# Kernel tuning notes

Hardware: AMD Instinct MI355X
Metric: run time of the kernel (lower is better)

Reference implementation:

```python
import jax, jax.numpy as jnp
import numpy as np

B, S, D, H = 2, 2048, 1024, 16
HD = D // H  # head dim = 64


def setup_inputs() -> dict:
    key = jax.random.key(0)
    ks = jax.random.split(key, 12)
    s = 1.0 / np.sqrt(D)
    return {
        "query": jax.random.normal(ks[0], (B, S, D), jnp.float32),
        "key": jax.random.normal(ks[1], (B, S, D), jnp.float32),
        "value": jax.random.normal(ks[2], (B, S, D), jnp.float32),
        "mask": jax.random.randint(ks[3], (B, S, S), 0, 2, jnp.int32),
        "wq_kernel": jax.random.normal(ks[4], (D, D), jnp.float32) * s,
        "wq_bias": jnp.zeros((D,), jnp.float32),
        "wk_kernel": jax.random.normal(ks[5], (D, D), jnp.float32) * s,
        "wk_bias": jnp.zeros((D,), jnp.float32),
        "wv_kernel": jax.random.normal(ks[6], (D, D), jnp.float32) * s,
        "wv_bias": jnp.zeros((D,), jnp.float32),
        "wo_kernel": jax.random.normal(ks[7], (D, D), jnp.float32) * s,
        "wo_bias": jnp.zeros((D,), jnp.float32),
    }


def reference(query, key, value, mask,
              wq_kernel, wq_bias, wk_kernel, wk_bias,
              wv_kernel, wv_bias, wo_kernel, wo_bias):
    b = query.shape[0]
    # Dense projections, then split heads: [B,S,D] -> [B,H,S,HD]
    def split_heads(x):
        return x.reshape(b, -1, H, HD).transpose(0, 2, 1, 3)

    q = split_heads(query @ wq_kernel + wq_bias)
    k = split_heads(key @ wk_kernel + wk_bias)
    v = split_heads(value @ wv_kernel + wv_bias)

    scores = jnp.einsum('bhqd,bhkd->bhqk', q, k) / jnp.sqrt(jnp.float32(HD))
    m = mask[:, None, :, :]  # [B,1,S,S] broadcast over heads
    scores = jnp.where(m == 0, jnp.float32(-1e9), scores)
    attn = jax.nn.softmax(scores, axis=-1)
    out = jnp.einsum('bhqk,bhkd->bhqd', attn, v)
    out = out.transpose(0, 2, 1, 3).reshape(b, -1, D)  # [B,S,D]
    return out @ wo_kernel + wo_bias
```

## Files before the change

### kernel.cpp

```cpp
#include <hip/hip_runtime.h>
#include <hip/hip_bf16.h>

typedef __attribute__((ext_vector_type(8))) short bf16x8;
typedef __attribute__((ext_vector_type(4))) float f32x4;
typedef __attribute__((ext_vector_type(16))) float f32x16;
typedef __attribute__((ext_vector_type(4))) unsigned int u32x4;
typedef unsigned long long u64;
typedef unsigned short u16;
typedef unsigned int u32;

#define LOG2E 1.44269504088896340736f

__device__ __forceinline__ u16 f2bf(float f) {
  u32 u = __builtin_bit_cast(u32, f);
  u32 r = u + 0x7FFFu + ((u >> 16) & 1u);
  return (u16)(r >> 16);
}

__device__ __forceinline__ u32 cvt_pk_bf16(float lo, float hi) {
  u32 r;
  asm("v_cvt_pk_bf16_f32 %0, %1, %2" : "=v"(r) : "v"(lo), "v"(hi));
  return r;
}

__device__ __forceinline__ void swap32(u32& a, u32& b) {
  asm("v_permlane32_swap_b32 %0, %1" : "+v"(a), "+v"(b));
}

__device__ __forceinline__ float fexp2(float x) {
#if __has_builtin(__builtin_amdgcn_exp2f)
  return __builtin_amdgcn_exp2f(x);
#else
  return exp2f(x);
#endif
}

__device__ __forceinline__ void gload16(const u16* g, u16* l) {
  __builtin_amdgcn_global_load_lds(
      (const __attribute__((address_space(1))) u32*)g,
      (__attribute__((address_space(3))) u32*)l, 16, 0, 0);
}

__global__ __launch_bounds__(256) void mask_bits(const int* __restrict__ mask,
                                                 u64* __restrict__ out) {
  const int nwords = 2 * 2048 * 32;
  int gw = (blockIdx.x * 256 + threadIdx.x) >> 6;
  int lane = threadIdx.x & 63;
  int nw = (gridDim.x * 256) >> 6;
  for (int w = gw; w < nwords; w += nw) {
    int m = mask[(size_t)w * 64 + lane];
    u64 bits = __ballot(m != 0);
    if (lane == 0) out[w] = bits;
  }
}

__global__ __launch_bounds__(256) void wtrans(const float* __restrict__ W0,
                                              const float* __restrict__ W1,
                                              const float* __restrict__ W2,
                                              const float* __restrict__ W3,
                                              u16* __restrict__ WtBase) {
  const float* W = (blockIdx.z == 0) ? W0 : (blockIdx.z == 1) ? W1
                    : (blockIdx.z == 2) ? W2 : W3;
  u16* T = WtBase + (size_t)blockIdx.z * 1048576;
  __shared__ float tile[32][33];
  int k0 = blockIdx.y * 32, n0 = blockIdx.x * 32;
  int tx = threadIdx.x, ty = threadIdx.y;
#pragma unroll
  for (int i = 0; i < 4; i++)
    tile[ty + i * 8][tx] = W[(size_t)(k0 + ty + i * 8) * 1024 + n0 + tx];
  __syncthreads();
#pragma unroll
  for (int i = 0; i < 4; i++)
    T[(size_t)(n0 + ty + i * 8) * 1024 + k0 + tx] = f2bf(tile[tx][ty + i * 8]);
}

__global__ __launch_bounds__(256) void vtrans(const u16* __restrict__ Vb,
                                              u16* __restrict__ Vt) {
  __shared__ u16 t[64][72];
  int bh = blockIdx.y, k0 = blockIdx.x * 64;
  const u16* src = Vb + (size_t)bh * 2048 * 64;
  u16* dst = Vt + (size_t)bh * 64 * 2048;
  int tid = threadIdx.x;
  int r = tid >> 2, c = (tid & 3) * 16;
  *(bf16x8*)&t[r][c] = *(const bf16x8*)(src + (size_t)(k0 + r) * 64 + c);
  *(bf16x8*)&t[r][c + 8] = *(const bf16x8*)(src + (size_t)(k0 + r) * 64 + c + 8);
  __syncthreads();
  int d = tid >> 2, kb = (tid & 3) * 16;
  u16 tmp[16];
#pragma unroll
  for (int i = 0; i < 16; i++) tmp[i] = t[kb + i][d];
  *(bf16x8*)(dst + (size_t)d * 2048 + k0 + kb) = *(bf16x8*)&tmp[0];
  *(bf16x8*)(dst + (size_t)d * 2048 + k0 + kb + 8) = *(bf16x8*)&tmp[8];
}

__global__ __launch_bounds__(256, 3) void gemm_qkv(
    const float* __restrict__ Aq, const float* __restrict__ Ak,
    const float* __restrict__ Av, const float* __restrict__ bq,
    const float* __restrict__ bk, const float* __restrict__ bv,
    const u16* __restrict__ WtBase, u16* __restrict__ OutBase) {
  constexpr int K = 1024;
  __shared__ alignas(16) u16 As[128][40];
  __shared__ alignas(16) u16 Bs[2][128][32];
  const int fid = blockIdx.x;
  const int c = fid & 7, i = fid >> 3;
  const int panel = c * 12 + (i >> 3);
  const int my = panel & 31, z = panel >> 5;
  const int m0 = my * 128, n0 = (i & 7) * 128;

  const float* A = (z == 0) ? Aq : (z == 1) ? Ak : Av;
  const float* bias = (z == 0) ? bq : (z == 1) ? bk : bv;
  const u16* Bt = WtBase + (size_t)z * 1048576;
  u16* Ob = OutBase + (size_t)z * 4194304;
  const float scale = (z == 0) ? 0.125f * LOG2E : 1.0f;

  const int tid = threadIdx.x;
  const int lane = tid & 63, wave = tid >> 6;
  const int wr = wave >> 1, wc = wave & 1;
  const int fr = lane & 15, fq = lane >> 4;

  const int arow = tid >> 1, ahalf = tid & 1;
  const float* Agp = A + (size_t)(m0 + arow) * K + ahalf * 16;
  const int srow = lane >> 2, scol = (lane & 3) * 8;
  const u16* Bgp = Bt + (size_t)(n0 + wave * 32 + srow) * K + scol;

  f32x4 acc[4][4];
#pragma unroll
  for (int i2 = 0; i2 < 4; i2++)
#pragma unroll
    for (int j = 0; j < 4; j++) acc[i2][j] = (f32x4){0.f, 0.f, 0.f, 0.f};

  gload16(Bgp, &Bs[0][wave * 32][0]);
  gload16(Bgp + 16 * K, &Bs[0][wave * 32 + 16][0]);
  float4 a0 = *(const float4*)(Agp);
  float4 a1 = *(const float4*)(Agp + 4);
  float4 a2 = *(const float4*)(Agp + 8);
  float4 a3 = *(const float4*)(Agp + 12);

  for (int k0 = 0; k0 < K; k0 += 32) {
    const int cur = (k0 >> 5) & 1;
    __builtin_amdgcn_sched_barrier(0);
    __builtin_amdgcn_s_barrier();
    __builtin_amdgcn_sched_barrier(0);
    u32 c0 = cvt_pk_bf16(a0.x, a0.y), c1 = cvt_pk_bf16(a0.z, a0.w);
    u32 c2 = cvt_pk_bf16(a1.x, a1.y), c3 = cvt_pk_bf16(a1.z, a1.w);
    u32 c4 = cvt_pk_bf16(a2.x, a2.y), c5 = cvt_pk_bf16(a2.z, a2.w);
    u32 c6 = cvt_pk_bf16(a3.x, a3.y), c7 = cvt_pk_bf16(a3.z, a3.w);
    *(u32x4*)&As[arow][ahalf * 16] = (u32x4){c0, c1, c2, c3};
    *(u32x4*)&As[arow][ahalf * 16 + 8] = (u32x4){c4, c5, c6, c7};
    if (k0 + 32 < K) {
      gload16(Bgp + k0 + 32, &Bs[cur ^ 1][wave * 32][0]);
      gload16(Bgp + k0 + 32 + 16 * K, &Bs[cur ^ 1][wave * 32 + 16][0]);
    }
    asm volatile("s_waitcnt lgkmcnt(0)" ::: "memory");
    __builtin_amdgcn_sched_barrier(0);
    __builtin_amdgcn_s_barrier();
    __builtin_amdgcn_sched_barrier(0);
    if (k0 + 32 < K) {
      a0 = *(const float4*)(Agp + k0 + 32);
      a1 = *(const float4*)(Agp + k0 + 36);
      a2 = *(const float4*)(Agp + k0 + 40);
      a3 = *(const float4*)(Agp + k0 + 44);
    }
    bf16x8 af[4], bfv[4];
#pragma unroll
    for (int i2 = 0; i2 < 4; i2++) {
      af[i2] = *(const bf16x8*)&As[wr * 64 + i2 * 16 + fr][fq * 8];
      bfv[i2] = *(const bf16x8*)&Bs[cur][wc * 64 + i2 * 16 + fr][fq * 8];
    }
#pragma unroll
    for (int i2 = 0; i2 < 4; i2++)
#pragma unroll
      for (int j = 0; j < 4; j++)
        acc[i2][j] = __builtin_amdgcn_mfma_f32_16x16x32_bf16(af[i2], bfv[j],
                                                             acc[i2][j], 0, 0, 0);
  }
#pragma unroll
  for (int j = 0; j < 4; j++) {
    int col = n0 + wc * 64 + j * 16 + fr;
    float bcol = bias[col];
    int hh = col >> 6, hd = col & 63;
#pragma unroll
    for (int i2 = 0; i2 < 4; i2++) {
#pragma unroll
      for (int r = 0; r < 4; r++) {
        int row = m0 + wr * 64 + i2 * 16 + fq * 4 + r;
        int bb = row >> 11, ss = row & 2047;
        float val = (acc[i2][j][r] + bcol) * scale;
        Ob[(((size_t)bb * 16 + hh) * 2048 + ss) * 64 + hd] = f2bf(val);
      }
    }
  }
}

__global__ __launch_bounds__(256, 2) void gemm_out(const u16* __restrict__ A,
                                                   const u16* __restrict__ Bt,
                                                   const float* __restrict__ bias,
                                                   float* __restrict__ Out) {
  constexpr int K = 1024;
  __shared__ alignas(16) u16 As[64][32];
  __shared__ alignas(16) u16 Bs[128][32];
  const int fid = blockIdx.x;
  const int c = fid & 7, i = fid >> 3;
  const int panel = c * 8 + (i >> 3);
  const int m0 = panel * 64, n0 = (i & 7) * 128;

  const int tid = threadIdx.x;
  const int lane = tid & 63, wave = tid >> 6;
  const int wr = wave >> 1, wc = wave & 1;
  const int fr = lane & 15, fq = lane >> 4;

  const int srow = lane >> 2, scol = (lane & 3) * 8;
  const u16* Agp = A + (size_t)(m0 + wave * 16 + srow) * K + scol;
  const u16* Bgp = Bt + (size_t)(n0 + wave * 32 + srow) * K + scol;
  u16* As0 = &As[wave * 16][0];
  u16* Bs0 = &Bs[wave * 32][0];
  u16* Bs1 = &Bs[wave * 32 + 16][0];

  f32x4 acc[2][4];
#pragma unroll
  for (int i2 = 0; i2 < 2; i2++)
#pragma unroll
    for (int j = 0; j < 4; j++) acc[i2][j] = (f32x4){0.f, 0.f, 0.f, 0.f};

  for (int k0 = 0; k0 < K; k0 += 32) {
    gload16(Agp + k0, As0);
    gload16(Bgp + k0, Bs0);
    gload16(Bgp + k0 + 16 * K, Bs1);
    __syncthreads();
    bf16x8 af[2], bfv[4];
#pragma unroll
    for (int i2 = 0; i2 < 2; i2++)
      af[i2] = *(const bf16x8*)&As[wr * 32 + i2 * 16 + fr][fq * 8];
#pragma unroll
    for (int j = 0; j < 4; j++)
      bfv[j] = *(const bf16x8*)&Bs[wc * 64 + j * 16 + fr][fq * 8];
#pragma unroll
    for (int i2 = 0; i2 < 2; i2++)
#pragma unroll
      for (int j = 0; j < 4; j++)
        acc[i2][j] = __builtin_amdgcn_mfma_f32_16x16x32_bf16(af[i2], bfv[j],
                                                             acc[i2][j], 0, 0, 0);
    __syncthreads();
  }
#pragma unroll
  for (int j = 0; j < 4; j++) {
    int col = n0 + wc * 64 + j * 16 + fr;
    float bcol = bias[col];
#pragma unroll
    for (int i2 = 0; i2 < 2; i2++) {
#pragma unroll
      for (int r = 0; r < 4; r++) {
        int row = m0 + wr * 32 + i2 * 16 + fq * 4 + r;
        Out[(size_t)row * 1024 + col] = acc[i2][j][r] + bcol;
      }
    }
  }
}

__global__ __launch_bounds__(512, 4) void attn(const u16* __restrict__ Qb,
                                               const u16* __restrict__ Kb,
                                               const u16* __restrict__ Vtb,
                                               const u64* __restrict__ mbits,
                                               u16* __restrict__ AO) {
  const int fid = blockIdx.x;
  const int nfid = ((fid & 7) << 6) + (fid >> 3);
  const int qt = nfid & 15, bh = nfid >> 4;
  const int h = bh & 15, b = bh >> 4;
  const int q0 = qt * 128;
  const u16* Qh = Qb + (size_t)bh * 2048 * 64;
  const u16* Kh = Kb + (size_t)bh * 2048 * 64;
  const u16* Vh = Vtb + (size_t)bh * 64 * 2048;

  __shared__ alignas(16) u16 smem[32768];
  const int tid = threadIdx.x, lane = tid & 63, wave = tid >> 6;
  const int qw = wave >> 1, kg = wave & 1;
  const int ql = lane & 31, hi = lane >> 5;
  const int l3 = (lane >> 3) & 7, l7 = lane & 7;
  const int srcoff = (l7 ^ l3) * 8;
  const int swz = ql & 7;

  u16* KBg = smem + kg * 8192;
  u16* VBg = smem + 16384 + kg * 8192;
  const int row0 = qw * 16 + l3;

  {
    const u16* ksrc = Kh + (size_t)(kg * 64 + row0) * 64 + srcoff;
    u16* kdst = KBg + (qw * 16) * 64;
    gload16(ksrc, kdst);
    gload16(ksrc + 8 * 64, kdst + 8 * 64);
    const u16* vsrc = Vh + (size_t)row0 * 2048 + kg * 64 + srcoff;
    u16* vdst = VBg + (qw * 16) * 64;
    gload16(vsrc, vdst);
    gload16(vsrc + 8 * 2048, vdst + 8 * 64);
  }
  const int q = q0 + qw * 32 + ql;
  bf16x8 qf[4];
  {
    const u16* qp = Qh + (size_t)q * 64 + hi * 8;
#pragma unroll
    for (int kd = 0; kd < 4; kd++) qf[kd] = *(const bf16x8*)(qp + kd * 16);
  }
  f32x16 accO0, accO1;
#pragma unroll
  for (int i = 0; i < 16; i++) {
    accO0[i] = 0.f;
    accO1[i] = 0.f;
  }
  float lrun = 0.f;
  const u64* mrow = mbits + ((size_t)b * 2048 + q) * 32;
  const u16* kpre = Kh + (size_t)((kg + 2) * 64 + row0) * 64 + srcoff;
  const u16* vpre = Vh + (size_t)row0 * 2048 + (kg + 2) * 64 + srcoff;
  u64 wcur = mrow[kg];
  __syncthreads();

  for (int r = 0; r < 16; r++) {
    const int cur = r & 1;
    const u16* KBc = KBg + cur * 4096;
    const u16* VBc = VBg + cur * 4096;
    u64 wnxt = 0;
    if (r < 15) {
      u16* kdst = KBg + (cur ^ 1) * 4096 + (qw * 16) * 64;
      gload16(kpre, kdst);
      gload16(kpre + 8 * 64, kdst + 8 * 64);
      u16* vdst = VBg + (cur ^ 1) * 4096 + (qw * 16) * 64;
      gload16(vpre, vdst);
      gload16(vpre + 8 * 2048, vdst + 8 * 64);
      kpre += 8192;
      vpre += 128;
      wnxt = mrow[2 * r + kg + 2];
    }
    const u32 wlo = (u32)wcur, wh = (u32)(wcur >> 32);
    bf16x8 pf[4];
    float rs = 0.f;

    {
      f32x16 sf;
#pragma unroll
      for (int g = 0; g < 4; g++) {
        u32 nib = (wlo >> (8 * g + 4 * hi)) & 0xFu;
        sf[4 * g + 0] = (nib & 1u) ? 0.f : -1024.f;
        sf[4 * g + 1] = (nib & 2u) ? 0.f : -1024.f;
        sf[4 * g + 2] = (nib & 4u) ? 0.f : -1024.f;
        sf[4 * g + 3] = (nib & 8u) ? 0.f : -1024.f;
      }
      __builtin_amdgcn_s_setprio(1);
#pragma unroll
      for (int kd = 0; kd < 4; kd++) {
        bf16x8 kf = *(const bf16x8*)&KBc[ql * 64 + ((2 * kd + hi) ^ swz) * 8];
        sf = __builtin_amdgcn_mfma_f32_32x32x16_bf16(kf, qf[kd], sf, 0, 0, 0);
      }
      __builtin_amdgcn_s_setprio(0);
#pragma unroll
      for (int i = 0; i < 16; i++) {
        sf[i] = fexp2(sf[i]);
        rs += sf[i];
      }
      u32 a0 = cvt_pk_bf16(sf[0], sf[1]), a1 = cvt_pk_bf16(sf[2], sf[3]);
      u32 b0 = cvt_pk_bf16(sf[4], sf[5]), b1 = cvt_pk_bf16(sf[6], sf[7]);
      swap32(a0, b0);
      swap32(a1, b1);
      pf[0] = __builtin_bit_cast(bf16x8, (u32x4){a0, a1, b0, b1});
      u32 c0 = cvt_pk_bf16(sf[8], sf[9]), c1 = cvt_pk_bf16(sf[10], sf[11]);
      u32 d0 = cvt_pk_bf16(sf[12], sf[13]), d1 = cvt_pk_bf16(sf[14], sf[15]);
      swap32(c0, d0);
      swap32(c1, d1);
      pf[1] = __builtin_bit_cast(bf16x8, (u32x4){c0, c1, d0, d1});
    }
    {
      f32x16 sf;
#pragma unroll
      for (int g = 0; g < 4; g++) {
        u32 nib = (wh >> (8 * g + 4 * hi)) & 0xFu;
        sf[4 * g + 0] = (nib & 1u) ? 0.f : -1024.f;
        sf[4 * g + 1] = (nib & 2u) ? 0.f : -1024.f;
        sf[4 * g + 2] = (nib & 4u) ? 0.f : -1024.f;
        sf[4 * g + 3] = (nib & 8u) ? 0.f : -1024.f;
      }
      __builtin_amdgcn_s_setprio(1);
#pragma unroll
      for (int kd = 0; kd < 4; kd++) {
        bf16x8 kf =
            *(const bf16x8*)&KBc[(32 + ql) * 64 + ((2 * kd + hi) ^ swz) * 8];
        sf = __builtin_amdgcn_mfma_f32_32x32x16_bf16(kf, qf[kd], sf, 0, 0, 0);
      }
      __builtin_amdgcn_s_setprio(0);
#pragma unroll
      for (int i = 0; i < 16; i++) {
        sf[i] = fexp2(sf[i]);
        rs += sf[i];
      }
      u32 a0 = cvt_pk_bf16(sf[0], sf[1]), a1 = cvt_pk_bf16(sf[2], sf[3]);
      u32 b0 = cvt_pk_bf16(sf[4], sf[5]), b1 = cvt_pk_bf16(sf[6], sf[7]);
      swap32(a0, b0);
      swap32(a1, b1);
      pf[2] = __builtin_bit_cast(bf16x8, (u32x4){a0, a1, b0, b1});
      u32 c0 = cvt_pk_bf16(sf[8], sf[9]), c1 = cvt_pk_bf16(sf[10], sf[11]);
      u32 d0 = cvt_pk_bf16(sf[12], sf[13]), d1 = cvt_pk_bf16(sf[14], sf[15]);
      swap32(c0, d0);
      swap32(c1, d1);
      pf[3] = __builtin_bit_cast(bf16x8, (u32x4){c0, c1, d0, d1});
    }
    rs += __shfl_xor(rs, 32);
    lrun += rs;

    __builtin_amdgcn_s_setprio(1);
#pragma unroll
    for (int ks = 0; ks < 4; ks++) {
      bf16x8 vf0 = *(const bf16x8*)&VBc[ql * 64 + ((2 * ks + hi) ^ swz) * 8];
      bf16x8 vf1 =
          *(const bf16x8*)&VBc[(32 + ql) * 64 + ((2 * ks + hi) ^ swz) * 8];
      accO0 = __builtin_amdgcn_mfma_f32_32x32x16_bf16(vf0, pf[ks], accO0, 0, 0, 0);
      accO1 = __builtin_amdgcn_mfma_f32_32x32x16_bf16(vf1, pf[ks], accO1, 0, 0, 0);
    }
    __builtin_amdgcn_s_setprio(0);
    wcur = wnxt;
    __syncthreads();
  }

  float* MO = (float*)smem;
  float* ML = (float*)((char*)smem + 32768);
  u16* OT = smem + 18432;
  if (kg == 1) {
#pragma unroll
    for (int i = 0; i < 16; i++) {
      int d = (i & 3) + 8 * (i >> 2) + 4 * hi;
      MO[(qw * 64 + d) * 32 + ql] = accO0[i];
      MO[(qw * 64 + 32 + d) * 32 + ql] = accO1[i];
    }
    if (hi == 0) ML[qw * 32 + ql] = lrun;
  }
  __syncthreads();
  if (kg == 0) {
#pragma unroll
    for (int i = 0; i < 16; i++) {
      int d = (i & 3) + 8 * (i >> 2) + 4 * hi;
      accO0[i] += MO[(qw * 64 + d) * 32 + ql];
      accO1[i] += MO[(qw * 64 + 32 + d) * 32 + ql];
    }
    lrun += ML[qw * 32 + ql];
    float inv = 1.f / fmaxf(lrun, 1e-30f);
    const int orow = qw * 32 + ql;
#pragma unroll
    for (int s = 0; s < 8; s++) {
      int d0 = (2 * s & 3) + 8 * (s >> 1) + 4 * hi;
      u32 p0 = cvt_pk_bf16(accO0[2 * s] * inv, accO0[2 * s + 1] * inv);
      u32 p1 = cvt_pk_bf16(accO1[2 * s] * inv, accO1[2 * s + 1] * inv);
      *(u32*)&OT[orow * 72 + d0] = p0;
      *(u32*)&OT[orow * 72 + 32 + d0] = p1;
    }
  }
  __syncthreads();
  {
    int rq = tid >> 2, c0 = (tid & 3) * 16;
    const u16* src = &OT[rq * 72 + c0];
    u16* dst = AO + ((size_t)(b * 2048 + q0 + rq)) * 1024 + h * 64 + c0;
    *(bf16x8*)(dst) = *(const bf16x8*)(src);
    *(bf16x8*)(dst + 8) = *(const bf16x8*)(src + 8);
  }
}

extern "C" void kernel_launch(void* const* d_in, const int* in_sizes, int n_in,
                              void* d_out, int out_size, void* d_ws,
                              size_t ws_size, hipStream_t stream) {
  const float* q = (const float*)d_in[0];
  const float* k = (const float*)d_in[1];
  const float* v = (const float*)d_in[2];
  const int* mask = (const int*)d_in[3];
  const float* wq = (const float*)d_in[4];
  const float* bq = (const float*)d_in[5];
  const float* wk = (const float*)d_in[6];
  const float* bk = (const float*)d_in[7];
  const float* wv = (const float*)d_in[8];
  const float* bv = (const float*)d_in[9];
  const float* wo = (const float*)d_in[10];
  const float* bo = (const float*)d_in[11];

  char* ws = (char*)d_ws;
  u16* Wt = (u16*)(ws);
  u16* Qb = (u16*)(ws + (size_t)(8u << 20));
  u16* Kb = (u16*)(ws + (size_t)(16u << 20));
  u16* Vb = (u16*)(ws + (size_t)(24u << 20));
  u16* AO = (u16*)(ws + (size_t)(32u << 20));
  u64* mb = (u64*)(ws + (size_t)(40u << 20));
  u16* Vt = (u16*)(ws + (size_t)(41u << 20));

  wtrans<<<dim3(32, 32, 4), dim3(32, 8), 0, stream>>>(wq, wk, wv, wo, Wt);
  gemm_qkv<<<dim3(768), dim3(256), 0, stream>>>(q, k, v, bq, bk, bv, Wt, Qb);
  mask_bits<<<dim3(2048), dim3(256), 0, stream>>>(mask, mb);
  vtrans<<<dim3(32, 32), dim3(256), 0, stream>>>(Vb, Vt);
  attn<<<dim3(512), dim3(512), 0, stream>>>(Qb, Kb, Vt, mb, AO);
  gemm_out<<<dim3(512), dim3(256), 0, stream>>>(AO, Wt + 3 * 1048576, bo,
                                                (float*)d_out);
}
```

Baseline: 132.7 us.

## Unroll projection GEMM K-loop by two with deeper A register prefetch

Result: slower. 137.1 us (+3.3%).

```diff
diff --git a/kernel.cpp b/kernel.cpp
--- a/kernel.cpp
+++ b/kernel.cpp
@@ -131,48 +131,101 @@
 
   gload16(Bgp, &Bs[0][wave * 32][0]);
   gload16(Bgp + 16 * K, &Bs[0][wave * 32 + 16][0]);
-  float4 a0 = *(const float4*)(Agp);
-  float4 a1 = *(const float4*)(Agp + 4);
-  float4 a2 = *(const float4*)(Agp + 8);
-  float4 a3 = *(const float4*)(Agp + 12);
-
-  for (int k0 = 0; k0 < K; k0 += 32) {
-    const int cur = (k0 >> 5) & 1;
+  float4 aA0 = *(const float4*)(Agp);
+  float4 aA1 = *(const float4*)(Agp + 4);
+  float4 aA2 = *(const float4*)(Agp + 8);
+  float4 aA3 = *(const float4*)(Agp + 12);
+  float4 aB0 = *(const float4*)(Agp + 32);
+  float4 aB1 = *(const float4*)(Agp + 36);
+  float4 aB2 = *(const float4*)(Agp + 40);
+  float4 aB3 = *(const float4*)(Agp + 44);
+
+  for (int k0 = 0; k0 < K; k0 += 64) {
     __builtin_amdgcn_sched_barrier(0);
     __builtin_amdgcn_s_barrier();
     __builtin_amdgcn_sched_barrier(0);
-    u32 c0 = cvt_pk_bf16(a0.x, a0.y), c1 = cvt_pk_bf16(a0.z, a0.w);
-    u32 c2 = cvt_pk_bf16(a1.x, a1.y), c3 = cvt_pk_bf16(a1.z, a1.w);
-    u32 c4 = cvt_pk_bf16(a2.x, a2.y), c5 = cvt_pk_bf16(a2.z, a2.w);
-    u32 c6 = cvt_pk_bf16(a3.x, a3.y), c7 = cvt_pk_bf16(a3.z, a3.w);
-    *(u32x4*)&As[arow][ahalf * 16] = (u32x4){c0, c1, c2, c3};
-    *(u32x4*)&As[arow][ahalf * 16 + 8] = (u32x4){c4, c5, c6, c7};
-    if (k0 + 32 < K) {
-      gload16(Bgp + k0 + 32, &Bs[cur ^ 1][wave * 32][0]);
-      gload16(Bgp + k0 + 32 + 16 * K, &Bs[cur ^ 1][wave * 32 + 16][0]);
-    }
+    {
+      u32 c0 = cvt_pk_bf16(aA0.x, aA0.y), c1 = cvt_pk_bf16(aA0.z, aA0.w);
+      u32 c2 = cvt_pk_bf16(aA1.x, aA1.y), c3 = cvt_pk_bf16(aA1.z, aA1.w);
+      u32 c4 = cvt_pk_bf16(aA2.x, aA2.y), c5 = cvt_pk_bf16(aA2.z, aA2.w);
+      u32 c6 = cvt_pk_bf16(aA3.x, aA3.y), c7 = cvt_pk_bf16(aA3.z, aA3.w);
+      *(u32x4*)&As[arow][ahalf * 16] = (u32x4){c0, c1, c2, c3};
+      *(u32x4*)&As[arow][ahalf * 16 + 8] = (u32x4){c4, c5, c6, c7};
+    }
+    gload16(Bgp + k0 + 32, &Bs[1][wave * 32][0]);
+    gload16(Bgp + k0 + 32 + 16 * K, &Bs[1][wave * 32 + 16][0]);
     asm volatile("s_waitcnt lgkmcnt(0)" ::: "memory");
     __builtin_amdgcn_sched_barrier(0);
     __builtin_amdgcn_s_barrier();
     __builtin_amdgcn_sched_barrier(0);
-    if (k0 + 32 < K) {
-      a0 = *(const float4*)(Agp + k0 + 32);
-      a1 = *(const float4*)(Agp + k0 + 36);
-      a2 = *(const float4*)(Agp + k0 + 40);
-      a3 = *(const float4*)(Agp + k0 + 44);
-    }
-    bf16x8 af[4], bfv[4];
-#pragma unroll
-    for (int i2 = 0; i2 < 4; i2++) {
-      af[i2] = *(const bf16x8*)&As[wr * 64 + i2 * 16 + fr][fq * 8];
-      bfv[i2] = *(const bf16x8*)&Bs[cur][wc * 64 + i2 * 16 + fr][fq * 8];
-    }
-#pragma unroll
-    for (int i2 = 0; i2 < 4; i2++)
-#pragma unroll
-      for (int j = 0; j < 4; j++)
-        acc[i2][j] = __builtin_amdgcn_mfma_f32_16x16x32_bf16(af[i2], bfv[j],
-                                                             acc[i2][j], 0, 0, 0);
+    {
+      int ka = (k0 + 64 < K) ? k0 + 64 : 0;
+      aA0 = *(const float4*)(Agp + ka);
+      aA1 = *(const float4*)(Agp + ka + 4);
+      aA2 = *(const float4*)(Agp + ka + 8);
+      aA3 = *(const float4*)(Agp + ka + 12);
+    }
+    __builtin_amdgcn_sched_barrier(0);
+    asm volatile("s_waitcnt vmcnt(10)" ::: "memory");
+    __builtin_amdgcn_sched_barrier(0);
+    {
+      bf16x8 af[4], bfv[4];
+#pragma unroll
+      for (int i2 = 0; i2 < 4; i2++) {
+        af[i2] = *(const bf16x8*)&As[wr * 64 + i2 * 16 + fr][fq * 8];
+        bfv[i2] = *(const bf16x8*)&Bs[0][wc * 64 + i2 * 16 + fr][fq * 8];
+      }
+#pragma unroll
+      for (int i2 = 0; i2 < 4; i2++)
+#pragma unroll
+        for (int j = 0; j < 4; j++)
+          acc[i2][j] = __builtin_amdgcn_mfma_f32_16x16x32_bf16(
+              af[i2], bfv[j], acc[i2][j], 0, 0, 0);
+    }
+    __builtin_amdgcn_sched_barrier(0);
+    __builtin_amdgcn_s_barrier();
+    __builtin_amdgcn_sched_barrier(0);
+    {
+      u32 c0 = cvt_pk_bf16(aB0.x, aB0.y), c1 = cvt_pk_bf16(aB0.z, aB0.w);
+      u32 c2 = cvt_pk_bf16(aB1.x, aB1.y), c3 = cvt_pk_bf16(aB1.z, aB1.w);
+      u32 c4 = cvt_pk_bf16(aB2.x, aB2.y), c5 = cvt_pk_bf16(aB2.z, aB2.w);
+      u32 c6 = cvt_pk_bf16(aB3.x, aB3.y), c7 = cvt_pk_bf16(aB3.z, aB3.w);
+      *(u32x4*)&As[arow][ahalf * 16] = (u32x4){c0, c1, c2, c3};
+      *(u32x4*)&As[arow][ahalf * 16 + 8] = (u32x4){c4, c5, c6, c7};
+    }
+    {
+      int kb = (k0 + 64 < K) ? k0 + 64 : 0;
+      gload16(Bgp + kb, &Bs[0][wave * 32][0]);
+      gload16(Bgp + kb + 16 * K, &Bs[0][wave * 32 + 16][0]);
+    }
+    asm volatile("s_waitcnt lgkmcnt(0)" ::: "memory");
+    __builtin_amdgcn_sched_barrier(0);
+    __builtin_amdgcn_s_barrier();
+    __builtin_amdgcn_sched_barrier(0);
+    {
+      int ka = (k0 + 96 < K) ? k0 + 96 : 0;
+      aB0 = *(const float4*)(Agp + ka);
+      aB1 = *(const float4*)(Agp + ka + 4);
+      aB2 = *(const float4*)(Agp + ka + 8);
+      aB3 = *(const float4*)(Agp + ka + 12);
+    }
+    __builtin_amdgcn_sched_barrier(0);
+    asm volatile("s_waitcnt vmcnt(10)" ::: "memory");
+    __builtin_amdgcn_sched_barrier(0);
+    {
+      bf16x8 af[4], bfv[4];
+#pragma unroll
+      for (int i2 = 0; i2 < 4; i2++) {
+        af[i2] = *(const bf16x8*)&As[wr * 64 + i2 * 16 + fr][fq * 8];
+        bfv[i2] = *(const bf16x8*)&Bs[1][wc * 64 + i2 * 16 + fr][fq * 8];
+      }
+#pragma unroll
+      for (int i2 = 0; i2 < 4; i2++)
+#pragma unroll
+        for (int j = 0; j < 4; j++)
+          acc[i2][j] = __builtin_amdgcn_mfma_f32_16x16x32_bf16(
+              af[i2], bfv[j], acc[i2][j], 0, 0, 0);
+    }
   }
 #pragma unroll
   for (int j = 0; j < 4; j++) {
```
